# Kernel tuning notes

Measured on AMD Instinct MI355X. Metric: run time of the kernel, lower is better.

## Reference

```python
import jax, jax.numpy as jnp
import numpy as np

H = 1024      # hidden_size
VIN = 32000   # input_size (source vocab)
VOUT = 32000  # output_size (target vocab)
S = 256       # src length
T = 256       # trg length


def setup_inputs() -> dict:
    key = jax.random.key(0)
    ks = jax.random.split(key, 16)
    def n(k, shape):
        return jax.random.normal(k, shape, dtype=jnp.float32) * 0.02
    return {
        "src": jax.random.randint(ks[0], (S,), 0, VIN, dtype=jnp.int32),
        "trg": jax.random.randint(ks[1], (T,), 0, VOUT, dtype=jnp.int32),
        "start": jnp.zeros((1,), dtype=jnp.int32),
        "enc_emb": n(ks[2], (VIN, H)),
        "enc_Wih": n(ks[3], (4 * H, H)),
        "enc_Whh": n(ks[4], (4 * H, H)),
        "enc_bih": n(ks[5], (4 * H,)),
        "enc_bhh": n(ks[6], (4 * H,)),
        "dec_emb": n(ks[7], (VOUT, H)),
        "dec_Wih": n(ks[8], (4 * H, H)),
        "dec_Whh": n(ks[9], (4 * H, H)),
        "dec_bih": n(ks[10], (4 * H,)),
        "dec_bhh": n(ks[11], (4 * H,)),
        "lin_W": n(ks[12], (VOUT, H)),
        "lin_b": n(ks[13], (VOUT,)),
    }


def _lstm_cell(x, h, c, Wih, Whh, bih, bhh):
    # PyTorch gate order: input, forget, cell(g), output
    gates = x @ Wih.T + bih + h @ Whh.T + bhh  # [4H]
    i, f, g, o = jnp.split(gates, 4)
    i = jax.nn.sigmoid(i)
    f = jax.nn.sigmoid(f)
    g = jnp.tanh(g)
    o = jax.nn.sigmoid(o)
    c = f * c + i * g
    h = o * jnp.tanh(c)
    return h, c


def reference(src, trg, start, enc_emb, enc_Wih, enc_Whh, enc_bih, enc_bhh,
              dec_emb, dec_Wih, dec_Whh, dec_bih, dec_bhh, lin_W, lin_b):
    hdim = enc_Wih.shape[1]
    h0 = jnp.zeros((hdim,), dtype=enc_emb.dtype)

    # --- encoder: scan over src tokens (batch=1, unbatched state) ---
    enc_x = enc_emb[src]  # [S, H]
    def estep(carry, x):
        h, c = carry
        h, c = _lstm_cell(x, h, c, enc_Wih, enc_Whh, enc_bih, enc_bhh)
        return (h, c), None
    (h, c), _ = jax.lax.scan(estep, (h0, h0), enc_x)

    # --- decoder: teacher forcing ratio 1 -> input is start, trg[:-1] ---
    dec_in = jnp.concatenate([start, trg[:-1]])  # [T]
    dec_x = dec_emb[dec_in]  # [T, H]
    def dstep(carry, x):
        h, c = carry
        h, c = _lstm_cell(x, h, c, dec_Wih, dec_Whh, dec_bih, dec_bhh)
        logits = h @ lin_W.T + lin_b  # [VOUT]  (dropout p=0 is identity)
        return (h, c), jax.nn.log_softmax(logits)
    _, pred = jax.lax.scan(dstep, (h, c), dec_x)
    return pred  # [T, VOUT]
```

## Files before the change

### kernel.cpp

```cpp
#include <hip/hip_runtime.h>
#include <hip/hip_bf16.h>


#define HDIM 1024
#define SLEN 256
#define TLEN 256
#define VOUTN 32000
#define G4 4096
#define NWGC 128
#define HPW 8

typedef __bf16 bf16_t;
typedef __bf16 bf16x8 __attribute__((ext_vector_type(8)));
typedef float f32x4 __attribute__((ext_vector_type(4)));
typedef unsigned long long u64;

static __device__ inline bf16x8 cvt8(float4 a, float4 b) {
    bf16x8 r;
    r[0] = (__bf16)a.x; r[1] = (__bf16)a.y; r[2] = (__bf16)a.z; r[3] = (__bf16)a.w;
    r[4] = (__bf16)b.x; r[5] = (__bf16)b.y; r[6] = (__bf16)b.z; r[7] = (__bf16)b.w;
    return r;
}

__global__ __launch_bounds__(256) void input_gemm(
    const float* __restrict__ emb,
    const int* __restrict__ toks,
    const int* __restrict__ start,
    const float* __restrict__ W,
    const float* __restrict__ bih,
    const float* __restrict__ bhh,
    float* __restrict__ out)
{
    __shared__ int stok[SLEN];
    int tid = threadIdx.x;
    {
        int t = tid;
        int tok;
        if (start) tok = (t == 0) ? start[0] : toks[t - 1];
        else       tok = toks[t];
        stok[t] = tok;
    }
    __syncthreads();

    int wave = tid >> 6, lane = tid & 63;
    int l15 = lane & 15, quad = lane >> 4;
    int n = (blockIdx.x * 4 + wave) * 16 + l15;
    const float* wrow = W + (size_t)n * HDIM + quad * 8;

    f32x4 acc[16] = {};
    for (int kt = 0; kt < HDIM / 32; ++kt) {
        float4 b0 = *(const float4*)(wrow + kt * 32);
        float4 b1 = *(const float4*)(wrow + kt * 32 + 4);
        bf16x8 bf = cvt8(b0, b1);
#pragma unroll
        for (int mt = 0; mt < 16; ++mt) {
            const float* arow = emb + (size_t)stok[mt * 16 + l15] * HDIM + kt * 32 + quad * 8;
            bf16x8 af = cvt8(*(const float4*)arow, *(const float4*)(arow + 4));
            acc[mt] = __builtin_amdgcn_mfma_f32_16x16x32_bf16(af, bf, acc[mt], 0, 0, 0);
        }
    }
    float bias = bih[n] + bhh[n];
#pragma unroll
    for (int mt = 0; mt < 16; ++mt)
#pragma unroll
        for (int r = 0; r < 4; ++r) {
            int t = mt * 16 + quad * 4 + r;
            out[(size_t)t * G4 + n] = acc[mt][r] + bias;
        }
}

__global__ __launch_bounds__(256, 1) void lstm_seq(
    const float* __restrict__ encXW,
    const float* __restrict__ decXW,
    const float* __restrict__ encWhh,
    const float* __restrict__ decWhh,
    u64* __restrict__ hseq,
    bf16_t* __restrict__ Hs)
{
    __shared__ float sh[HDIM + HDIM / 32];
    __shared__ float sg[32];

    const int tid = threadIdx.x;
    const int wg = blockIdx.x;
    const int wave = tid >> 6, lane = tid & 63;
    const int rg = (wave << 1) | (lane >> 5);
    const int ks = lane & 31;
    const int j0 = wg * HPW;

    float4 w[4][8];
    auto load_w = [&](const float* __restrict__ Wsrc) {
#pragma unroll
        for (int r = 0; r < 4; ++r) {
            int lr = rg * 4 + r;
            const float* src = Wsrc + (size_t)((lr >> 3) * HDIM + j0 + (lr & 7)) * HDIM + ks * 32;
#pragma unroll
            for (int i = 0; i < 8; ++i) w[r][i] = *(const float4*)(src + i * 4);
        }
    };
    load_w(encWhh);

    float creg = 0.f;

    for (int t = 0; t < SLEN + TLEN; ++t) {
        if (t == SLEN) load_w(decWhh);

        const float* xw = (t < SLEN) ? encXW + (size_t)t * G4
                                     : decXW + (size_t)(t - SLEN) * G4;
        float xg0 = 0.f, xg1 = 0.f, xg2 = 0.f, xg3 = 0.f;
        if (tid < HPW) {
            int j = j0 + tid;
            xg0 = xw[0 * HDIM + j];
            xg1 = xw[1 * HDIM + j];
            xg2 = xw[2 * HDIM + j];
            xg3 = xw[3 * HDIM + j];
        }

        const int k = tid << 2;
        const int pad = k >> 5;
        if (t == 0) {
            sh[k + pad]     = 0.f;
            sh[k + pad + 1] = 0.f;
            sh[k + pad + 2] = 0.f;
            sh[k + pad + 3] = 0.f;
        } else {
            const u64* hin = hseq + (size_t)t * HDIM + k;
            const unsigned tag = (unsigned)t;
            u64 v0, v1, v2, v3;
            for (;;) {
                v0 = __hip_atomic_load(hin + 0, __ATOMIC_RELAXED, __HIP_MEMORY_SCOPE_AGENT);
                v1 = __hip_atomic_load(hin + 1, __ATOMIC_RELAXED, __HIP_MEMORY_SCOPE_AGENT);
                v2 = __hip_atomic_load(hin + 2, __ATOMIC_RELAXED, __HIP_MEMORY_SCOPE_AGENT);
                v3 = __hip_atomic_load(hin + 3, __ATOMIC_RELAXED, __HIP_MEMORY_SCOPE_AGENT);
                if ((unsigned)(v0 >> 32) == tag && (unsigned)(v1 >> 32) == tag &&
                    (unsigned)(v2 >> 32) == tag && (unsigned)(v3 >> 32) == tag) break;
                __builtin_amdgcn_s_sleep(1);
            }
            sh[k + pad]     = __uint_as_float((unsigned)v0);
            sh[k + pad + 1] = __uint_as_float((unsigned)v1);
            sh[k + pad + 2] = __uint_as_float((unsigned)v2);
            sh[k + pad + 3] = __uint_as_float((unsigned)v3);
        }
        __syncthreads();

        float hv[32];
#pragma unroll
        for (int i = 0; i < 32; ++i) hv[i] = sh[ks * 33 + i];

        float s0 = 0.f, s1 = 0.f, s2 = 0.f, s3 = 0.f;
#pragma unroll
        for (int i = 0; i < 8; ++i) {
            float hx = hv[4 * i], hy = hv[4 * i + 1], hz = hv[4 * i + 2], hw = hv[4 * i + 3];
            s0 += w[0][i].x * hx + w[0][i].y * hy + w[0][i].z * hz + w[0][i].w * hw;
            s1 += w[1][i].x * hx + w[1][i].y * hy + w[1][i].z * hz + w[1][i].w * hw;
            s2 += w[2][i].x * hx + w[2][i].y * hy + w[2][i].z * hz + w[2][i].w * hw;
            s3 += w[3][i].x * hx + w[3][i].y * hy + w[3][i].z * hz + w[3][i].w * hw;
        }
        float ss[4] = {s0, s1, s2, s3};
#pragma unroll
        for (int r = 0; r < 4; ++r) {
            float s = ss[r];
            s += __shfl_down(s, 16, 32);
            s += __shfl_down(s, 8, 32);
            s += __shfl_down(s, 4, 32);
            s += __shfl_down(s, 2, 32);
            s += __shfl_down(s, 1, 32);
            if (ks == 0) sg[rg * 4 + r] = s;
        }
        __syncthreads();

        if (tid < HPW) {
            int j = j0 + tid;
            float gi = sg[0 * 8 + tid] + xg0;
            float gf = sg[1 * 8 + tid] + xg1;
            float gg = sg[2 * 8 + tid] + xg2;
            float go = sg[3 * 8 + tid] + xg3;
            float ii = 1.f / (1.f + expf(-gi));
            float ff = 1.f / (1.f + expf(-gf));
            float g  = tanhf(gg);
            float oo = 1.f / (1.f + expf(-go));
            float cn = ff * creg + ii * g;
            float hn = oo * tanhf(cn);
            creg = cn;
            if (t >= SLEN) Hs[(size_t)(t - SLEN) * HDIM + j] = (bf16_t)hn;
            if (t < SLEN + TLEN - 1) {
                u64 pk = ((u64)(unsigned)(t + 1) << 32) | (u64)__float_as_uint(hn);
                __hip_atomic_store(hseq + (size_t)(t + 1) * HDIM + j, pk,
                                   __ATOMIC_RELAXED, __HIP_MEMORY_SCOPE_AGENT);
            }
        }
    }
}

__global__ __launch_bounds__(256) void out_gemm(
    const bf16_t* __restrict__ Hs,
    const float* __restrict__ W,
    const float* __restrict__ bias,
    float* __restrict__ out)
{
    int tid = threadIdx.x;
    int wave = tid >> 6, lane = tid & 63;
    int l15 = lane & 15, quad = lane >> 4;
    int n = (blockIdx.x * 4 + wave) * 16 + l15;
    const float* wrow = W + (size_t)n * HDIM + quad * 8;

    f32x4 acc[16] = {};
    for (int kt = 0; kt < HDIM / 32; ++kt) {
        float4 b0 = *(const float4*)(wrow + kt * 32);
        float4 b1 = *(const float4*)(wrow + kt * 32 + 4);
        bf16x8 bf = cvt8(b0, b1);
#pragma unroll
        for (int mt = 0; mt < 16; ++mt) {
            bf16x8 af = *(const bf16x8*)(Hs + (size_t)(mt * 16 + l15) * HDIM + kt * 32 + quad * 8);
            acc[mt] = __builtin_amdgcn_mfma_f32_16x16x32_bf16(af, bf, acc[mt], 0, 0, 0);
        }
    }
    float bv = bias[n];
#pragma unroll
    for (int mt = 0; mt < 16; ++mt)
#pragma unroll
        for (int r = 0; r < 4; ++r) {
            int t = mt * 16 + quad * 4 + r;
            out[(size_t)t * VOUTN + n] = acc[mt][r] + bv;
        }
}

__global__ __launch_bounds__(256) void log_softmax_k(float* __restrict__ out)
{
    float* row = out + (size_t)blockIdx.x * VOUTN;
    int tid = threadIdx.x;
    int wave = tid >> 6, lane = tid & 63;
    __shared__ float sm[4], ss[4];

    float m = -1e30f;
    for (int i = tid; i < VOUTN; i += 256) m = fmaxf(m, row[i]);
    for (int o = 32; o; o >>= 1) m = fmaxf(m, __shfl_down(m, o, 64));
    if (lane == 0) sm[wave] = m;
    __syncthreads();
    float bm = fmaxf(fmaxf(sm[0], sm[1]), fmaxf(sm[2], sm[3]));

    float s = 0.f;
    for (int i = tid; i < VOUTN; i += 256) s += expf(row[i] - bm);
    for (int o = 32; o; o >>= 1) s += __shfl_down(s, o, 64);
    if (lane == 0) ss[wave] = s;
    __syncthreads();
    float lse = bm + logf(ss[0] + ss[1] + ss[2] + ss[3]);

    for (int i = tid; i < VOUTN; i += 256) row[i] -= lse;
}

extern "C" void kernel_launch(void* const* d_in, const int* in_sizes, int n_in,
                              void* d_out, int out_size, void* d_ws, size_t ws_size,
                              hipStream_t stream) {
    const int*   src     = (const int*)d_in[0];
    const int*   trg     = (const int*)d_in[1];
    const int*   start   = (const int*)d_in[2];
    const float* enc_emb = (const float*)d_in[3];
    const float* enc_Wih = (const float*)d_in[4];
    const float* enc_Whh = (const float*)d_in[5];
    const float* enc_bih = (const float*)d_in[6];
    const float* enc_bhh = (const float*)d_in[7];
    const float* dec_emb = (const float*)d_in[8];
    const float* dec_Wih = (const float*)d_in[9];
    const float* dec_Whh = (const float*)d_in[10];
    const float* dec_bih = (const float*)d_in[11];
    const float* dec_bhh = (const float*)d_in[12];
    const float* lin_W   = (const float*)d_in[13];
    const float* lin_b   = (const float*)d_in[14];
    float* out = (float*)d_out;

    char* ws = (char*)d_ws;
    float*  encXW = (float*)(ws);
    float*  decXW = (float*)(ws + 4194304);
    bf16_t* Hs    = (bf16_t*)(ws + 8388608);
    u64*    hseq  = (u64*)(ws + 9437184);

    hipMemsetAsync(hseq, 0, (size_t)(SLEN + TLEN) * HDIM * sizeof(u64), stream);

    input_gemm<<<64, 256, 0, stream>>>(enc_emb, src, nullptr, enc_Wih, enc_bih, enc_bhh, encXW);
    input_gemm<<<64, 256, 0, stream>>>(dec_emb, trg, start,   dec_Wih, dec_bih, dec_bhh, decXW);

    lstm_seq<<<NWGC, 256, 0, stream>>>(encXW, decXW, enc_Whh, dec_Whh, hseq, Hs);

    out_gemm<<<500, 256, 0, stream>>>(Hs, lin_W, lin_b, out);
    log_softmax_k<<<256, 256, 0, stream>>>(out);
}
```

Baseline: 2.522 ms.

## Merge input GEMMs with hseq clearing, wave-0 polling, fast math, vectorized softmax

```diff
diff --git a/kernel.cpp b/kernel.cpp
--- a/kernel.cpp
+++ b/kernel.cpp
@@ -22,29 +22,45 @@
     return r;
 }
 
-__global__ __launch_bounds__(256) void input_gemm(
-    const float* __restrict__ emb,
-    const int* __restrict__ toks,
+static __device__ inline float sig_f(float x) {
+    return 1.f / (1.f + __expf(-x));
+}
+static __device__ inline float tanh_f(float x) {
+    float e = __expf(-2.f * fabsf(x));
+    float r = (1.f - e) / (1.f + e);
+    return copysignf(r, x);
+}
+
+__global__ __launch_bounds__(64) void xw_all(
+    const int* __restrict__ src, const int* __restrict__ trg,
     const int* __restrict__ start,
-    const float* __restrict__ W,
-    const float* __restrict__ bih,
-    const float* __restrict__ bhh,
-    float* __restrict__ out)
+    const float* __restrict__ enc_emb, const float* __restrict__ enc_Wih,
+    const float* __restrict__ enc_bih, const float* __restrict__ enc_bhh,
+    const float* __restrict__ dec_emb, const float* __restrict__ dec_Wih,
+    const float* __restrict__ dec_bih, const float* __restrict__ dec_bhh,
+    float* __restrict__ encXW, float* __restrict__ decXW,
+    u64* __restrict__ hseq)
 {
+    const int b = blockIdx.x, tid = threadIdx.x;
+
+    for (size_t i = (size_t)b * 64 + tid; i < (size_t)512 * 1024; i += (size_t)512 * 64)
+        hseq[i] = 0ULL;
+
+    const bool enc = (b < 256);
+    const int*   toks = enc ? src : trg;
+    const float* emb  = enc ? enc_emb : dec_emb;
+    const float* W    = enc ? enc_Wih : dec_Wih;
+    const float* bi   = enc ? enc_bih : dec_bih;
+    const float* bh   = enc ? enc_bhh : dec_bhh;
+    float*       outp = enc ? encXW : decXW;
+
     __shared__ int stok[SLEN];
-    int tid = threadIdx.x;
-    {
-        int t = tid;
-        int tok;
-        if (start) tok = (t == 0) ? start[0] : toks[t - 1];
-        else       tok = toks[t];
-        stok[t] = tok;
-    }
+    for (int i = tid; i < SLEN; i += 64)
+        stok[i] = enc ? toks[i] : (i == 0 ? start[0] : toks[i - 1]);
     __syncthreads();
 
-    int wave = tid >> 6, lane = tid & 63;
-    int l15 = lane & 15, quad = lane >> 4;
-    int n = (blockIdx.x * 4 + wave) * 16 + l15;
+    const int l15 = tid & 15, quad = tid >> 4;
+    const int n = (b & 255) * 16 + l15;
     const float* wrow = W + (size_t)n * HDIM + quad * 8;
 
     f32x4 acc[16] = {};
@@ -54,18 +70,18 @@
         bf16x8 bf = cvt8(b0, b1);
 #pragma unroll
         for (int mt = 0; mt < 16; ++mt) {
-            const float* arow = emb + (size_t)stok[mt * 16 + l15] * HDIM + kt * 32 + quad * 8;
-            bf16x8 af = cvt8(*(const float4*)arow, *(const float4*)(arow + 4));
+            const float* ar = emb + (size_t)stok[mt * 16 + l15] * HDIM + kt * 32 + quad * 8;
+            bf16x8 af = cvt8(*(const float4*)ar, *(const float4*)(ar + 4));
             acc[mt] = __builtin_amdgcn_mfma_f32_16x16x32_bf16(af, bf, acc[mt], 0, 0, 0);
         }
     }
-    float bias = bih[n] + bhh[n];
+    float bias = bi[n] + bh[n];
 #pragma unroll
     for (int mt = 0; mt < 16; ++mt)
 #pragma unroll
         for (int r = 0; r < 4; ++r) {
             int t = mt * 16 + quad * 4 + r;
-            out[(size_t)t * G4 + n] = acc[mt][r] + bias;
+            outp[(size_t)t * G4 + n] = acc[mt][r] + bias;
         }
 }
 
@@ -92,9 +108,9 @@
 #pragma unroll
         for (int r = 0; r < 4; ++r) {
             int lr = rg * 4 + r;
-            const float* src = Wsrc + (size_t)((lr >> 3) * HDIM + j0 + (lr & 7)) * HDIM + ks * 32;
-#pragma unroll
-            for (int i = 0; i < 8; ++i) w[r][i] = *(const float4*)(src + i * 4);
+            const float* srcp = Wsrc + (size_t)((lr >> 3) * HDIM + j0 + (lr & 7)) * HDIM + ks * 32;
+#pragma unroll
+            for (int i = 0; i < 8; ++i) w[r][i] = *(const float4*)(srcp + i * 4);
         }
     };
     load_w(encWhh);
@@ -104,43 +120,61 @@
     for (int t = 0; t < SLEN + TLEN; ++t) {
         if (t == SLEN) load_w(decWhh);
 
-        const float* xw = (t < SLEN) ? encXW + (size_t)t * G4
-                                     : decXW + (size_t)(t - SLEN) * G4;
+        if (wave == 0) {
+            if (t == 0) {
+#pragma unroll
+                for (int i = 0; i < 8; ++i) {
+                    int j = lane * 8 + i;        sh[j + (j >> 5)] = 0.f;
+                    int j2 = 512 + lane * 8 + i; sh[j2 + (j2 >> 5)] = 0.f;
+                }
+            } else {
+                const u64* row = hseq + (size_t)t * HDIM;
+                const unsigned tag = (unsigned)t;
+                const u64* pa = row + lane * 8;
+                const u64* pb = row + 512 + lane * 8;
+                for (;;) {
+                    u64 a0 = __hip_atomic_load(pa, __ATOMIC_RELAXED, __HIP_MEMORY_SCOPE_AGENT);
+                    u64 b0 = __hip_atomic_load(pb, __ATOMIC_RELAXED, __HIP_MEMORY_SCOPE_AGENT);
+                    if (__all(((unsigned)(a0 >> 32) == tag) && ((unsigned)(b0 >> 32) == tag)))
+                        break;
+                }
+                u64 av[8], bv[8];
+                for (;;) {
+#pragma unroll
+                    for (int i = 0; i < 8; ++i)
+                        av[i] = __hip_atomic_load(pa + i, __ATOMIC_RELAXED, __HIP_MEMORY_SCOPE_AGENT);
+#pragma unroll
+                    for (int i = 0; i < 8; ++i)
+                        bv[i] = __hip_atomic_load(pb + i, __ATOMIC_RELAXED, __HIP_MEMORY_SCOPE_AGENT);
+                    bool ok = true;
+#pragma unroll
+                    for (int i = 0; i < 8; ++i)
+                        ok = ok && ((unsigned)(av[i] >> 32) == tag)
+                                && ((unsigned)(bv[i] >> 32) == tag);
+                    if (__all(ok)) break;
+                    __builtin_amdgcn_s_sleep(1);
+                }
+#pragma unroll
+                for (int i = 0; i < 8; ++i) {
+                    int j = lane * 8 + i;
+                    sh[j + (j >> 5)] = __uint_as_float((unsigned)av[i]);
+                    int j2 = 512 + lane * 8 + i;
+                    sh[j2 + (j2 >> 5)] = __uint_as_float((unsigned)bv[i]);
+                }
+            }
+        }
+        __syncthreads();
+
         float xg0 = 0.f, xg1 = 0.f, xg2 = 0.f, xg3 = 0.f;
         if (tid < HPW) {
+            const float* xw = (t < SLEN) ? encXW + (size_t)t * G4
+                                         : decXW + (size_t)(t - SLEN) * G4;
             int j = j0 + tid;
             xg0 = xw[0 * HDIM + j];
             xg1 = xw[1 * HDIM + j];
             xg2 = xw[2 * HDIM + j];
             xg3 = xw[3 * HDIM + j];
         }
-
-        const int k = tid << 2;
-        const int pad = k >> 5;
-        if (t == 0) {
-            sh[k + pad]     = 0.f;
-            sh[k + pad + 1] = 0.f;
-            sh[k + pad + 2] = 0.f;
-            sh[k + pad + 3] = 0.f;
-        } else {
-            const u64* hin = hseq + (size_t)t * HDIM + k;
-            const unsigned tag = (unsigned)t;
-            u64 v0, v1, v2, v3;
-            for (;;) {
-                v0 = __hip_atomic_load(hin + 0, __ATOMIC_RELAXED, __HIP_MEMORY_SCOPE_AGENT);
-                v1 = __hip_atomic_load(hin + 1, __ATOMIC_RELAXED, __HIP_MEMORY_SCOPE_AGENT);
-                v2 = __hip_atomic_load(hin + 2, __ATOMIC_RELAXED, __HIP_MEMORY_SCOPE_AGENT);
-                v3 = __hip_atomic_load(hin + 3, __ATOMIC_RELAXED, __HIP_MEMORY_SCOPE_AGENT);
-                if ((unsigned)(v0 >> 32) == tag && (unsigned)(v1 >> 32) == tag &&
-                    (unsigned)(v2 >> 32) == tag && (unsigned)(v3 >> 32) == tag) break;
-                __builtin_amdgcn_s_sleep(1);
-            }
-            sh[k + pad]     = __uint_as_float((unsigned)v0);
-            sh[k + pad + 1] = __uint_as_float((unsigned)v1);
-            sh[k + pad + 2] = __uint_as_float((unsigned)v2);
-            sh[k + pad + 3] = __uint_as_float((unsigned)v3);
-        }
-        __syncthreads();
 
         float hv[32];
 #pragma unroll
@@ -174,12 +208,12 @@
             float gf = sg[1 * 8 + tid] + xg1;
             float gg = sg[2 * 8 + tid] + xg2;
             float go = sg[3 * 8 + tid] + xg3;
-            float ii = 1.f / (1.f + expf(-gi));
-            float ff = 1.f / (1.f + expf(-gf));
-            float g  = tanhf(gg);
-            float oo = 1.f / (1.f + expf(-go));
+            float ii = sig_f(gi);
+            float ff = sig_f(gf);
+            float g  = tanh_f(gg);
+            float oo = sig_f(go);
             float cn = ff * creg + ii * g;
-            float hn = oo * tanhf(cn);
+            float hn = oo * tanh_f(cn);
             creg = cn;
             if (t >= SLEN) Hs[(size_t)(t - SLEN) * HDIM + j] = (bf16_t)hn;
             if (t < SLEN + TLEN - 1) {
@@ -224,28 +258,45 @@
         }
 }
 
-__global__ __launch_bounds__(256) void log_softmax_k(float* __restrict__ out)
+__global__ __launch_bounds__(1024) void log_softmax_k(float* __restrict__ out)
 {
     float* row = out + (size_t)blockIdx.x * VOUTN;
-    int tid = threadIdx.x;
-    int wave = tid >> 6, lane = tid & 63;
-    __shared__ float sm[4], ss[4];
+    float4* r4 = (float4*)row;
+    const int tid = threadIdx.x;
+    const int wave = tid >> 6, lane = tid & 63;
+    __shared__ float sred[16];
 
     float m = -1e30f;
-    for (int i = tid; i < VOUTN; i += 256) m = fmaxf(m, row[i]);
+    for (int i = tid; i < VOUTN / 4; i += 1024) {
+        float4 v = r4[i];
+        m = fmaxf(fmaxf(fmaxf(m, v.x), fmaxf(v.y, v.z)), v.w);
+    }
     for (int o = 32; o; o >>= 1) m = fmaxf(m, __shfl_down(m, o, 64));
-    if (lane == 0) sm[wave] = m;
+    if (lane == 0) sred[wave] = m;
     __syncthreads();
-    float bm = fmaxf(fmaxf(sm[0], sm[1]), fmaxf(sm[2], sm[3]));
+    float bm = sred[0];
+#pragma unroll
+    for (int i = 1; i < 16; ++i) bm = fmaxf(bm, sred[i]);
+    __syncthreads();
 
     float s = 0.f;
-    for (int i = tid; i < VOUTN; i += 256) s += expf(row[i] - bm);
+    for (int i = tid; i < VOUTN / 4; i += 1024) {
+        float4 v = r4[i];
+        s += __expf(v.x - bm) + __expf(v.y - bm) + __expf(v.z - bm) + __expf(v.w - bm);
+    }
     for (int o = 32; o; o >>= 1) s += __shfl_down(s, o, 64);
-    if (lane == 0) ss[wave] = s;
+    if (lane == 0) sred[wave] = s;
     __syncthreads();
-    float lse = bm + logf(ss[0] + ss[1] + ss[2] + ss[3]);
-
-    for (int i = tid; i < VOUTN; i += 256) row[i] -= lse;
+    float S = 0.f;
+#pragma unroll
+    for (int i = 0; i < 16; ++i) S += sred[i];
+    float lse = bm + __logf(S);
+
+    for (int i = tid; i < VOUTN / 4; i += 1024) {
+        float4 v = r4[i];
+        v.x -= lse; v.y -= lse; v.z -= lse; v.w -= lse;
+        r4[i] = v;
+    }
 }
 
 extern "C" void kernel_launch(void* const* d_in, const int* in_sizes, int n_in,
@@ -274,13 +325,13 @@
     bf16_t* Hs    = (bf16_t*)(ws + 8388608);
     u64*    hseq  = (u64*)(ws + 9437184);
 
-    hipMemsetAsync(hseq, 0, (size_t)(SLEN + TLEN) * HDIM * sizeof(u64), stream);
-
-    input_gemm<<<64, 256, 0, stream>>>(enc_emb, src, nullptr, enc_Wih, enc_bih, enc_bhh, encXW);
-    input_gemm<<<64, 256, 0, stream>>>(dec_emb, trg, start,   dec_Wih, dec_bih, dec_bhh, decXW);
+    xw_all<<<512, 64, 0, stream>>>(src, trg, start,
+                                   enc_emb, enc_Wih, enc_bih, enc_bhh,
+                                   dec_emb, dec_Wih, dec_bih, dec_bhh,
+                                   encXW, decXW, hseq);
 
     lstm_seq<<<NWGC, 256, 0, stream>>>(encXW, decXW, enc_Whh, dec_Whh, hseq, Hs);
 
     out_gemm<<<500, 256, 0, stream>>>(Hs, lin_W, lin_b, out);
-    log_softmax_k<<<256, 256, 0, stream>>>(out);
-}
+    log_softmax_k<<<256, 1024, 0, stream>>>(out);
+}
```

After: 2.297 ms. -8.9%, faster.
